# Kernel optimization log

Hardware: AMD Instinct MI355X
Metric: run time of the kernel (lower is better)

Reference implementation:

```python
import math
import jax, jax.numpy as jnp
import numpy as np

N_HEAD = 16
ROPE_BASE = 10000.0


def _rope_sin_cos(T, head_size, dtype):
    half = head_size // 2
    pos = jnp.arange(T, dtype=jnp.float32)[:, None]                      # [T,1]
    div = jnp.exp(jnp.arange(0, head_size, 2, dtype=jnp.float32) * (-math.log(ROPE_BASE) / head_size))  # [half]
    ang = pos * div                                                       # [T,half]
    return jnp.sin(ang).astype(dtype), jnp.cos(ang).astype(dtype)


def _apply_rope(q, k, sin, cos):
    # q,k: [B,T,H,D]; sin,cos: [T,D/2] -> broadcast [1,T,1,D/2]
    half = q.shape[-1] // 2
    sin = sin[None, :, None, :]
    cos = cos[None, :, None, :]
    q1, q2 = q[..., :half], q[..., half:]
    k1, k2 = k[..., :half], k[..., half:]
    q_rot = jnp.concatenate([q1 * cos - q2 * sin, q2 * cos + q1 * sin], axis=-1)
    k_rot = jnp.concatenate([k1 * cos - k2 * sin, k2 * cos + k1 * sin], axis=-1)
    return q_rot, k_rot


def setup_inputs() -> dict:
    key = jax.random.key(0)
    k1, k2, k3 = jax.random.split(key, 3)
    B, T, C = 2, 2048, 2048
    x = jax.random.normal(k1, (B, T, C), dtype=jnp.float32)
    qkv_w = jax.random.normal(k2, (3 * C, C), dtype=jnp.float32) * 0.02
    out_w = jax.random.normal(k3, (C, C), dtype=jnp.float32) * 0.02
    return {"x": x, "qkv_w": qkv_w, "out_w": out_w}


def reference(x, qkv_w, out_w):
    B, T, C = x.shape
    H = N_HEAD
    D = C // H
    qkv = (x @ qkv_w.T).reshape(B, T, 3, H, D)
    q, k, v = qkv[:, :, 0], qkv[:, :, 1], qkv[:, :, 2]   # [B,T,H,D]
    sin, cos = _rope_sin_cos(T, D, x.dtype)
    q, k = _apply_rope(q, k, sin, cos)
    scale = 1.0 / math.sqrt(D)
    scores = jnp.einsum('bthd,bshd->bhts', q, k) * scale  # [B,H,T,T]
    causal = jnp.tril(jnp.ones((T, T), dtype=bool))
    scores = jnp.where(causal[None, None], scores, jnp.finfo(scores.dtype).min)
    probs = jax.nn.softmax(scores, axis=-1)
    attn = jnp.einsum('bhts,bshd->bthd', probs, v)        # [B,T,H,D] (flash output layout)
    # Faithful to original: view(B,T,H,D).permute(0,2,1,3).reshape(B,T,C)
    attn = jnp.transpose(attn, (0, 2, 1, 3)).reshape(B, T, C)
    return attn @ out_w.T
```

## Files before the change

kernel.cpp:

```cpp
#include <hip/hip_runtime.h>

typedef __attribute__((ext_vector_type(8))) short short8;
typedef __attribute__((ext_vector_type(4))) float f32x4;

#define GLOAD16(g, l) __builtin_amdgcn_global_load_lds(                         \
    (const __attribute__((address_space(1))) void*)(g),                          \
    (__attribute__((address_space(3))) void*)(l), 16, 0, 0)

__device__ __forceinline__ float bf2f(unsigned short u) {
  union { unsigned int i; float f; } c; c.i = ((unsigned int)u) << 16; return c.f;
}
__device__ __forceinline__ unsigned short f2bf(float f) {
  union { float f; unsigned int i; } c; c.f = f;
  unsigned int u = c.i;
  u = (u + 0x7fffu + ((u >> 16) & 1u)) >> 16;
  return (unsigned short)u;
}

__global__ __launch_bounds__(256) void cvt_f32_bf16(const float* __restrict__ src,
                                                    unsigned short* __restrict__ dst,
                                                    int n8) {
  int i = blockIdx.x * 256 + threadIdx.x;
  if (i >= n8) return;
  const float4* s4 = (const float4*)src + (long)i * 2;
  float4 a = s4[0], b = s4[1];
  short8 o;
  o[0] = (short)f2bf(a.x); o[1] = (short)f2bf(a.y);
  o[2] = (short)f2bf(a.z); o[3] = (short)f2bf(a.w);
  o[4] = (short)f2bf(b.x); o[5] = (short)f2bf(b.y);
  o[6] = (short)f2bf(b.z); o[7] = (short)f2bf(b.w);
  *((short8*)dst + i) = o;
}

template<int OUT_F32>
__global__ __launch_bounds__(256) void gemm_bt(const unsigned short* __restrict__ A,
                                               const unsigned short* __restrict__ B,
                                               void* __restrict__ Cout,
                                               int M, int N, int K) {
  __shared__ __attribute__((aligned(16))) unsigned short Ah[128 * 64];
  __shared__ __attribute__((aligned(16))) unsigned short Bh[128 * 64];
  const int tid = threadIdx.x;
  const int l = tid & 63;
  const int w = tid >> 6;
  const int wm = w >> 1, wn = w & 1;
  const long brow = (long)blockIdx.y * 128;
  const long bcol = (long)blockIdx.x * 128;

  f32x4 acc[4][4];
#pragma unroll
  for (int i = 0; i < 4; ++i)
#pragma unroll
    for (int j = 0; j < 4; ++j) acc[i][j] = (f32x4){0.f, 0.f, 0.f, 0.f};

  const int srow = tid >> 3;
  const int sg = tid & 7;
  const int lwb = w << 10;

  for (int k0 = 0; k0 < K; k0 += 64) {
    __syncthreads();
#pragma unroll
    for (int i = 0; i < 4; ++i) {
      const int r = srow + i * 32;
      const int gp = (sg ^ (r & 7)) * 8;
      GLOAD16(A + (brow + r) * K + k0 + gp, (char*)Ah + lwb + i * 4096);
      GLOAD16(B + (bcol + r) * K + k0 + gp, (char*)Bh + lwb + i * 4096);
    }
    __syncthreads();
#pragma unroll
    for (int ks = 0; ks < 2; ++ks) {
      short8 af[4], bf[4];
#pragma unroll
      for (int mi = 0; mi < 4; ++mi) {
        const int row = wm * 64 + mi * 16 + (l & 15);
        const int byt = (row * 128 + (l >> 4) * 16 + ks * 64) ^ ((row & 7) << 4);
        af[mi] = *(const short8*)((const char*)Ah + byt);
      }
#pragma unroll
      for (int nj = 0; nj < 4; ++nj) {
        const int row = wn * 64 + nj * 16 + (l & 15);
        const int byt = (row * 128 + (l >> 4) * 16 + ks * 64) ^ ((row & 7) << 4);
        bf[nj] = *(const short8*)((const char*)Bh + byt);
      }
#pragma unroll
      for (int mi = 0; mi < 4; ++mi)
#pragma unroll
        for (int nj = 0; nj < 4; ++nj)
          acc[mi][nj] = __builtin_amdgcn_mfma_f32_16x16x32_bf16(af[mi], bf[nj],
                                                                acc[mi][nj], 0, 0, 0);
    }
  }

  const long rb = brow + wm * 64 + (l >> 4) * 4;
  const long cb = bcol + wn * 64 + (l & 15);
#pragma unroll
  for (int mi = 0; mi < 4; ++mi)
#pragma unroll
    for (int nj = 0; nj < 4; ++nj)
#pragma unroll
      for (int j = 0; j < 4; ++j) {
        const long row = rb + mi * 16 + j;
        const long col = cb + nj * 16;
        if (OUT_F32) ((float*)Cout)[row * N + col] = acc[mi][nj][j];
        else ((unsigned short*)Cout)[row * N + col] = f2bf(acc[mi][nj][j]);
      }
}

__global__ __launch_bounds__(256) void rope_qk(unsigned short* __restrict__ qkv) {
  int gid = blockIdx.x * 256 + threadIdx.x;
  int m = gid >> 10;
  int h = (gid >> 6) & 15;
  int d = gid & 63;
  int t = m & 2047;
  long base = (long)m * 6144 + h * 128;
  float inv = expf(-(float)(2 * d) * 0.07195578415606394f);
  float ang = (float)t * inv;
  float s = sinf(ang), c = cosf(ang);
  float q1 = bf2f(qkv[base + d]),        q2 = bf2f(qkv[base + 64 + d]);
  qkv[base + d]        = f2bf(q1 * c - q2 * s);
  qkv[base + 64 + d]   = f2bf(q2 * c + q1 * s);
  float k1 = bf2f(qkv[base + 2048 + d]), k2 = bf2f(qkv[base + 2048 + 64 + d]);
  qkv[base + 2048 + d]      = f2bf(k1 * c - k2 * s);
  qkv[base + 2048 + 64 + d] = f2bf(k2 * c + k1 * s);
}

__global__ __launch_bounds__(256) void transpose_v(const unsigned short* __restrict__ qkv,
                                                   unsigned short* __restrict__ vt) {
  __shared__ __attribute__((aligned(16))) unsigned short tile[32][136];
  int tid = threadIdx.x;
  int t0 = blockIdx.x * 32;
  int bh = blockIdx.y;
  int b = bh >> 4, h = bh & 15;
  {
    int tt = tid >> 3;
    int dcb = (tid & 7) * 16;
    const unsigned short* src = qkv + (long)(b * 2048 + t0 + tt) * 6144 + 4096 + h * 128 + dcb;
    *(short8*)&tile[tt][dcb]     = *(const short8*)src;
    *(short8*)&tile[tt][dcb + 8] = *(const short8*)(src + 8);
  }
  __syncthreads();
  {
    int d = tid >> 1;
    int ts = (tid & 1) * 16;
    short8 o0, o1;
#pragma unroll
    for (int i = 0; i < 8; ++i) o0[i] = (short)tile[ts + i][d];
#pragma unroll
    for (int i = 0; i < 8; ++i) o1[i] = (short)tile[ts + 8 + i][d];
    unsigned short* dst = vt + (long)bh * 262144 + (long)d * 2048 + t0 + ts;
    *(short8*)dst       = o0;
    *(short8*)(dst + 8) = o1;
  }
}

#define LOG2E 1.4426950408889634f
__global__ __launch_bounds__(256) void flash_attn(const unsigned short* __restrict__ qkv,
                                                  const unsigned short* __restrict__ vt,
                                                  unsigned short* __restrict__ attn) {
  __shared__ __attribute__((aligned(16))) unsigned short Kh[64 * 128];
  __shared__ __attribute__((aligned(16))) unsigned short Vh[128 * 64];
  __shared__ __attribute__((aligned(16))) unsigned short Ph[4][16 * 64];

  const int tid = threadIdx.x;
  const int l = tid & 63;
  const int w = tid >> 6;
  const int qt = (int)(gridDim.x - 1) - (int)blockIdx.x;
  const int bh = blockIdx.y;
  const int b = bh >> 4, h = bh & 15;
  const int q0 = qt * 64;
  const float scale = 0.08838834764831845f;

  short8 qf[4];
  {
    const int qrow = q0 + w * 16 + (l & 15);
    const unsigned short* qp = qkv + (long)(b * 2048 + qrow) * 6144 + h * 128 + (l >> 4) * 8;
#pragma unroll
    for (int dc = 0; dc < 4; ++dc) {
      short8 v = *(const short8*)(qp + dc * 32);
#pragma unroll
      for (int j = 0; j < 8; ++j) v[j] = (short)f2bf(bf2f((unsigned short)v[j]) * scale);
      qf[dc] = v;
    }
  }

  f32x4 accO[8];
#pragma unroll
  for (int i = 0; i < 8; ++i) accO[i] = (f32x4){0.f, 0.f, 0.f, 0.f};
  float mrow[4], lrow[4];
#pragma unroll
  for (int j = 0; j < 4; ++j) { mrow[j] = -INFINITY; lrow[j] = 0.f; }

  const int kvEnd = q0 + 64;
  for (int kv0 = 0; kv0 < kvEnd; kv0 += 64) {
    __syncthreads();
#pragma unroll
    for (int i = 0; i < 4; ++i) {
      const int kr = (tid >> 4) + i * 16;
      const int kgp = ((tid & 15) ^ (kr & 7)) * 8;
      GLOAD16(qkv + (long)(b * 2048 + kv0 + kr) * 6144 + 2048 + h * 128 + kgp,
              (char*)Kh + (w << 10) + i * 4096);
      const int vr = (tid >> 3) + i * 32;
      const int vgp = ((tid & 7) ^ (vr & 7)) * 8;
      GLOAD16(vt + (long)bh * 262144 + (long)vr * 2048 + kv0 + vgp,
              (char*)Vh + (w << 10) + i * 4096);
    }
    __syncthreads();

    f32x4 s[4];
#pragma unroll
    for (int kvt = 0; kvt < 4; ++kvt) {
      s[kvt] = (f32x4){0.f, 0.f, 0.f, 0.f};
#pragma unroll
      for (int dc = 0; dc < 4; ++dc) {
        const int krow = kvt * 16 + (l & 15);
        const int byt = (krow * 256 + (l >> 4) * 16 + dc * 64) ^ ((krow & 7) << 4);
        short8 kf = *(const short8*)((const char*)Kh + byt);
        s[kvt] = __builtin_amdgcn_mfma_f32_16x16x32_bf16(qf[dc], kf, s[kvt], 0, 0, 0);
      }
    }

    const int qrc = q0 + w * 16 + ((l >> 4) << 2);
    float mx[4];
#pragma unroll
    for (int j = 0; j < 4; ++j) mx[j] = -1e30f;
#pragma unroll
    for (int kvt = 0; kvt < 4; ++kvt) {
      const int kvcol = kv0 + kvt * 16 + (l & 15);
#pragma unroll
      for (int j = 0; j < 4; ++j) {
        float sv = s[kvt][j];
        if (kvcol > qrc + j) sv = -1e30f;
        s[kvt][j] = sv;
        mx[j] = fmaxf(mx[j], sv);
      }
    }
#pragma unroll
    for (int j = 0; j < 4; ++j) {
      float v = mx[j];
      v = fmaxf(v, __shfl_xor(v, 1));
      v = fmaxf(v, __shfl_xor(v, 2));
      v = fmaxf(v, __shfl_xor(v, 4));
      v = fmaxf(v, __shfl_xor(v, 8));
      mx[j] = v;
    }
    float alpha[4];
#pragma unroll
    for (int j = 0; j < 4; ++j) {
      float mnew = fmaxf(mrow[j], mx[j]);
      alpha[j] = exp2f((mrow[j] - mnew) * LOG2E);
      mrow[j] = mnew;
    }
    float ps[4] = {0.f, 0.f, 0.f, 0.f};
#pragma unroll
    for (int kvt = 0; kvt < 4; ++kvt) {
#pragma unroll
      for (int j = 0; j < 4; ++j) {
        float p = exp2f((s[kvt][j] - mrow[j]) * LOG2E);
        ps[j] += p;
        const int prow = ((l >> 4) << 2) + j;
        const int pcol = kvt * 16 + (l & 15);
        const int byt = (prow * 128 + pcol * 2) ^ ((prow & 7) << 4);
        *(unsigned short*)((char*)&Ph[w][0] + byt) = f2bf(p);
      }
    }
#pragma unroll
    for (int j = 0; j < 4; ++j) {
      float v = ps[j];
      v += __shfl_xor(v, 1);
      v += __shfl_xor(v, 2);
      v += __shfl_xor(v, 4);
      v += __shfl_xor(v, 8);
      lrow[j] = lrow[j] * alpha[j] + v;
    }
    __syncthreads();

#pragma unroll
    for (int dn = 0; dn < 8; ++dn)
#pragma unroll
      for (int j = 0; j < 4; ++j) accO[dn][j] *= alpha[j];
#pragma unroll
    for (int half = 0; half < 2; ++half) {
      const int prow = (l & 15);
      const int pbyt = (prow * 128 + (l >> 4) * 16 + half * 64) ^ ((prow & 7) << 4);
      short8 pf = *(const short8*)((const char*)&Ph[w][0] + pbyt);
#pragma unroll
      for (int dn = 0; dn < 8; ++dn) {
        const int vrow = dn * 16 + (l & 15);
        const int vbyt = (vrow * 128 + (l >> 4) * 16 + half * 64) ^ ((vrow & 7) << 4);
        short8 vf = *(const short8*)((const char*)Vh + vbyt);
        accO[dn] = __builtin_amdgcn_mfma_f32_16x16x32_bf16(pf, vf, accO[dn], 0, 0, 0);
      }
    }
  }

#pragma unroll
  for (int dn = 0; dn < 8; ++dn)
#pragma unroll
    for (int j = 0; j < 4; ++j) {
      const int qrow = q0 + w * 16 + ((l >> 4) << 2) + j;
      const int d = dn * 16 + (l & 15);
      attn[((long)bh * 2048 + qrow) * 128 + d] = f2bf(accO[dn][j] / lrow[j]);
    }
}

extern "C" void kernel_launch(void* const* d_in, const int* in_sizes, int n_in,
                              void* d_out, int out_size, void* d_ws, size_t ws_size,
                              hipStream_t stream) {
  (void)in_sizes; (void)n_in; (void)out_size; (void)ws_size;
  const float* x  = (const float*)d_in[0];
  const float* qw = (const float*)d_in[1];
  const float* ow = (const float*)d_in[2];
  float* out = (float*)d_out;
  char* ws = (char*)d_ws;

  unsigned short* xb    = (unsigned short*)(ws + 0);
  unsigned short* wqb   = (unsigned short*)(ws + 16777216);
  unsigned short* qkvb  = (unsigned short*)(ws + 41943040);
  unsigned short* vtb   = (unsigned short*)(ws + 0);
  unsigned short* attnb = (unsigned short*)(ws + 16777216);
  unsigned short* wob   = (unsigned short*)(ws + 33554432);

  cvt_f32_bf16<<<4096, 256, 0, stream>>>(x, xb, 1048576);
  cvt_f32_bf16<<<6144, 256, 0, stream>>>(qw, wqb, 1572864);
  gemm_bt<0><<<dim3(48, 32), 256, 0, stream>>>(xb, wqb, (void*)qkvb, 4096, 6144, 2048);
  cvt_f32_bf16<<<2048, 256, 0, stream>>>(ow, wob, 524288);
  rope_qk<<<16384, 256, 0, stream>>>(qkvb);
  transpose_v<<<dim3(64, 32), 256, 0, stream>>>(qkvb, vtb);
  flash_attn<<<dim3(32, 32), 256, 0, stream>>>(qkvb, vtb, attnb);
  gemm_bt<1><<<dim3(16, 32), 256, 0, stream>>>(attnb, wob, (void*)out, 4096, 2048, 2048);
}
```

Baseline: 505.5 us.

## Pair causal query tiles per block, double-buffer K/V, and table-based vectorized RoPE

Each flash-attention block now handles two query tiles, tile qtA and its mirror 31-qtA. The two tiles share K/V loads and balance the causal work across blocks. K/V staging is double-buffered: the next tile is prefetched with global_load_lds while the current one is computed, which leaves one __syncthreads per iteration. log2e is folded into the Q scale, so the per-element exp multiplies go away. RoPE now reads a precomputed sin/cos table with 8-wide vector loads instead of calling sin, cos and exp for every element. Register pressure grows from carrying two accumulator sets, and LDS use roughly doubles.

```diff
diff --git a/kernel.cpp b/kernel.cpp
--- a/kernel.cpp
+++ b/kernel.cpp
@@ -105,22 +105,51 @@
       }
 }
 
-__global__ __launch_bounds__(256) void rope_qk(unsigned short* __restrict__ qkv) {
+__global__ __launch_bounds__(256) void sincos_tab(float* __restrict__ tab) {
   int gid = blockIdx.x * 256 + threadIdx.x;
-  int m = gid >> 10;
-  int h = (gid >> 6) & 15;
-  int d = gid & 63;
-  int t = m & 2047;
-  long base = (long)m * 6144 + h * 128;
+  int t = gid >> 6, d = gid & 63;
   float inv = expf(-(float)(2 * d) * 0.07195578415606394f);
   float ang = (float)t * inv;
-  float s = sinf(ang), c = cosf(ang);
-  float q1 = bf2f(qkv[base + d]),        q2 = bf2f(qkv[base + 64 + d]);
-  qkv[base + d]        = f2bf(q1 * c - q2 * s);
-  qkv[base + 64 + d]   = f2bf(q2 * c + q1 * s);
-  float k1 = bf2f(qkv[base + 2048 + d]), k2 = bf2f(qkv[base + 2048 + 64 + d]);
-  qkv[base + 2048 + d]      = f2bf(k1 * c - k2 * s);
-  qkv[base + 2048 + 64 + d] = f2bf(k2 * c + k1 * s);
+  tab[2 * gid]     = sinf(ang);
+  tab[2 * gid + 1] = cosf(ang);
+}
+
+__global__ __launch_bounds__(256) void rope_qk(unsigned short* __restrict__ qkv,
+                                               const float* __restrict__ tab) {
+  int gid = blockIdx.x * 256 + threadIdx.x;
+  int m = gid >> 7;
+  int h = (gid >> 3) & 15;
+  int db = gid & 7;
+  int t = m & 2047;
+  long base = (long)m * 6144 + h * 128 + db * 8;
+  const float* tp = tab + ((long)(t << 6) + db * 8) * 2;
+  float4 t0 = *(const float4*)(tp + 0);
+  float4 t1 = *(const float4*)(tp + 4);
+  float4 t2 = *(const float4*)(tp + 8);
+  float4 t3 = *(const float4*)(tp + 12);
+  float sj[8] = {t0.x, t0.z, t1.x, t1.z, t2.x, t2.z, t3.x, t3.z};
+  float cj[8] = {t0.y, t0.w, t1.y, t1.w, t2.y, t2.w, t3.y, t3.w};
+
+  unsigned short* qp = qkv + base;
+  short8 q1 = *(short8*)qp, q2 = *(short8*)(qp + 64);
+  short8 o1, o2;
+#pragma unroll
+  for (int j = 0; j < 8; ++j) {
+    float a = bf2f((unsigned short)q1[j]), bq = bf2f((unsigned short)q2[j]);
+    o1[j] = (short)f2bf(a * cj[j] - bq * sj[j]);
+    o2[j] = (short)f2bf(bq * cj[j] + a * sj[j]);
+  }
+  *(short8*)qp = o1; *(short8*)(qp + 64) = o2;
+
+  unsigned short* kp = qkv + base + 2048;
+  short8 k1 = *(short8*)kp, k2 = *(short8*)(kp + 64);
+#pragma unroll
+  for (int j = 0; j < 8; ++j) {
+    float a = bf2f((unsigned short)k1[j]), bk = bf2f((unsigned short)k2[j]);
+    o1[j] = (short)f2bf(a * cj[j] - bk * sj[j]);
+    o2[j] = (short)f2bf(bk * cj[j] + a * sj[j]);
+  }
+  *(short8*)kp = o1; *(short8*)(kp + 64) = o2;
 }
 
 __global__ __launch_bounds__(256) void transpose_v(const unsigned short* __restrict__ qkv,
@@ -152,153 +181,176 @@
   }
 }
 
-#define LOG2E 1.4426950408889634f
-__global__ __launch_bounds__(256) void flash_attn(const unsigned short* __restrict__ qkv,
-                                                  const unsigned short* __restrict__ vt,
-                                                  unsigned short* __restrict__ attn) {
-  __shared__ __attribute__((aligned(16))) unsigned short Kh[64 * 128];
-  __shared__ __attribute__((aligned(16))) unsigned short Vh[128 * 64];
-  __shared__ __attribute__((aligned(16))) unsigned short Ph[4][16 * 64];
+#define STAGE(IT, BUF) do {                                                     \
+    const int kv0s_ = (IT) * 64;                                                \
+    _Pragma("unroll")                                                           \
+    for (int i_ = 0; i_ < 4; ++i_) {                                            \
+      const int kr_ = (tid >> 4) + i_ * 16;                                     \
+      const int kgp_ = ((tid & 15) ^ (kr_ & 7)) * 8;                            \
+      GLOAD16(qkv + (long)(b * 2048 + kv0s_ + kr_) * 6144 + 2048 + h * 128 + kgp_, \
+              (char*)&Kh[BUF][0] + (w << 10) + i_ * 4096);                      \
+      const int vr_ = (tid >> 3) + i_ * 32;                                     \
+      const int vgp_ = ((tid & 7) ^ (vr_ & 7)) * 8;                             \
+      GLOAD16(vt + (long)bh * 262144 + (long)vr_ * 2048 + kv0s_ + vgp_,         \
+              (char*)&Vh[BUF][0] + (w << 10) + i_ * 4096);                      \
+    }                                                                           \
+  } while (0)
+
+#define COMPUTE_TILE(QF, ACC, MR, LR, Q0, PHP, BUFB) do {                       \
+    f32x4 s_[4];                                                                \
+    _Pragma("unroll")                                                           \
+    for (int kvt_ = 0; kvt_ < 4; ++kvt_) {                                      \
+      s_[kvt_] = (f32x4){0.f, 0.f, 0.f, 0.f};                                   \
+      _Pragma("unroll")                                                         \
+      for (int dc_ = 0; dc_ < 4; ++dc_) {                                       \
+        const int krow_ = kvt_ * 16 + (l & 15);                                 \
+        const int byt_ = ((krow_ * 256 + (l >> 4) * 16 + dc_ * 64)              \
+                          ^ ((krow_ & 7) << 4)) + (BUFB);                       \
+        short8 kf_ = *(const short8*)((const char*)Kh + byt_);                  \
+        s_[kvt_] = __builtin_amdgcn_mfma_f32_16x16x32_bf16(QF[dc_], kf_,        \
+                                                           s_[kvt_], 0, 0, 0);  \
+      }                                                                         \
+    }                                                                           \
+    const int qrc_ = (Q0) + w * 16 + ((l >> 4) << 2);                           \
+    float mx_[4];                                                               \
+    _Pragma("unroll") for (int j_ = 0; j_ < 4; ++j_) mx_[j_] = -1e30f;          \
+    _Pragma("unroll")                                                           \
+    for (int kvt_ = 0; kvt_ < 4; ++kvt_) {                                      \
+      const int kvcol_ = kv0 + kvt_ * 16 + (l & 15);                            \
+      _Pragma("unroll")                                                         \
+      for (int j_ = 0; j_ < 4; ++j_) {                                          \
+        float sv_ = s_[kvt_][j_];                                               \
+        if (kvcol_ > qrc_ + j_) sv_ = -1e30f;                                   \
+        s_[kvt_][j_] = sv_;                                                     \
+        mx_[j_] = fmaxf(mx_[j_], sv_);                                          \
+      }                                                                         \
+    }                                                                           \
+    float alpha_[4];                                                            \
+    _Pragma("unroll")                                                           \
+    for (int j_ = 0; j_ < 4; ++j_) {                                            \
+      float v_ = mx_[j_];                                                       \
+      v_ = fmaxf(v_, __shfl_xor(v_, 1));                                        \
+      v_ = fmaxf(v_, __shfl_xor(v_, 2));                                        \
+      v_ = fmaxf(v_, __shfl_xor(v_, 4));                                        \
+      v_ = fmaxf(v_, __shfl_xor(v_, 8));                                        \
+      float mnew_ = fmaxf((MR)[j_], v_);                                        \
+      alpha_[j_] = exp2f((MR)[j_] - mnew_);                                     \
+      (MR)[j_] = mnew_;                                                         \
+    }                                                                           \
+    float ps_[4] = {0.f, 0.f, 0.f, 0.f};                                        \
+    _Pragma("unroll")                                                           \
+    for (int kvt_ = 0; kvt_ < 4; ++kvt_) {                                      \
+      _Pragma("unroll")                                                         \
+      for (int j_ = 0; j_ < 4; ++j_) {                                          \
+        float p_ = exp2f(s_[kvt_][j_] - (MR)[j_]);                              \
+        ps_[j_] += p_;                                                          \
+        const int prow_ = ((l >> 4) << 2) + j_;                                 \
+        const int pcol_ = kvt_ * 16 + (l & 15);                                 \
+        const int pb_ = (prow_ * 128 + pcol_ * 2) ^ ((prow_ & 7) << 4);         \
+        *(unsigned short*)((char*)(PHP) + pb_) = f2bf(p_);                      \
+      }                                                                         \
+    }                                                                           \
+    _Pragma("unroll")                                                           \
+    for (int j_ = 0; j_ < 4; ++j_) {                                            \
+      float v_ = ps_[j_];                                                       \
+      v_ += __shfl_xor(v_, 1);                                                  \
+      v_ += __shfl_xor(v_, 2);                                                  \
+      v_ += __shfl_xor(v_, 4);                                                  \
+      v_ += __shfl_xor(v_, 8);                                                  \
+      (LR)[j_] = (LR)[j_] * alpha_[j_] + v_;                                    \
+    }                                                                           \
+    asm volatile("s_waitcnt lgkmcnt(0)" ::: "memory");                          \
+    __builtin_amdgcn_sched_barrier(0);                                          \
+    _Pragma("unroll")                                                           \
+    for (int dn_ = 0; dn_ < 8; ++dn_)                                           \
+      _Pragma("unroll")                                                         \
+      for (int j_ = 0; j_ < 4; ++j_) (ACC)[dn_][j_] *= alpha_[j_];              \
+    _Pragma("unroll")                                                           \
+    for (int half_ = 0; half_ < 2; ++half_) {                                   \
+      const int prw_ = (l & 15);                                                \
+      const int pb_ = (prw_ * 128 + (l >> 4) * 16 + half_ * 64)                 \
+                      ^ ((prw_ & 7) << 4);                                      \
+      short8 pf_ = *(const short8*)((const char*)(PHP) + pb_);                  \
+      _Pragma("unroll")                                                         \
+      for (int dn_ = 0; dn_ < 8; ++dn_) {                                       \
+        const int vrow_ = dn_ * 16 + (l & 15);                                  \
+        const int vb_ = ((vrow_ * 128 + (l >> 4) * 16 + half_ * 64)             \
+                         ^ ((vrow_ & 7) << 4)) + (BUFB);                        \
+        short8 vf_ = *(const short8*)((const char*)Vh + vb_);                   \
+        (ACC)[dn_] = __builtin_amdgcn_mfma_f32_16x16x32_bf16(pf_, vf_,          \
+                                                             (ACC)[dn_], 0, 0, 0); \
+      }                                                                         \
+    }                                                                           \
+  } while (0)
+
+__global__ __launch_bounds__(256, 2) void flash_attn(const unsigned short* __restrict__ qkv,
+                                                     const unsigned short* __restrict__ vt,
+                                                     unsigned short* __restrict__ attn) {
+  __shared__ __attribute__((aligned(16))) unsigned short Kh[2][64 * 128];
+  __shared__ __attribute__((aligned(16))) unsigned short Vh[2][128 * 64];
+  __shared__ __attribute__((aligned(16))) unsigned short Ph[4][2][16 * 64];
 
   const int tid = threadIdx.x;
   const int l = tid & 63;
   const int w = tid >> 6;
-  const int qt = (int)(gridDim.x - 1) - (int)blockIdx.x;
   const int bh = blockIdx.y;
   const int b = bh >> 4, h = bh & 15;
-  const int q0 = qt * 64;
-  const float scale = 0.08838834764831845f;
-
-  short8 qf[4];
+  const int qtA = blockIdx.x;
+  const int qtB = 31 - qtA;
+  const int q0A = qtA * 64, q0B = qtB * 64;
+  const int endA = q0A + 64;
+  const int nIter = qtB + 1;
+  const float qscale = 0.08838834764831845f * 1.4426950408889634f;
+
+  short8 qfA[4], qfB[4];
   {
-    const int qrow = q0 + w * 16 + (l & 15);
-    const unsigned short* qp = qkv + (long)(b * 2048 + qrow) * 6144 + h * 128 + (l >> 4) * 8;
+    const int qrA = q0A + w * 16 + (l & 15);
+    const int qrB = q0B + w * 16 + (l & 15);
+    const unsigned short* qpA = qkv + (long)(b * 2048 + qrA) * 6144 + h * 128 + (l >> 4) * 8;
+    const unsigned short* qpB = qkv + (long)(b * 2048 + qrB) * 6144 + h * 128 + (l >> 4) * 8;
 #pragma unroll
     for (int dc = 0; dc < 4; ++dc) {
-      short8 v = *(const short8*)(qp + dc * 32);
-#pragma unroll
-      for (int j = 0; j < 8; ++j) v[j] = (short)f2bf(bf2f((unsigned short)v[j]) * scale);
-      qf[dc] = v;
+      short8 va = *(const short8*)(qpA + dc * 32);
+      short8 vb = *(const short8*)(qpB + dc * 32);
+#pragma unroll
+      for (int j = 0; j < 8; ++j) {
+        va[j] = (short)f2bf(bf2f((unsigned short)va[j]) * qscale);
+        vb[j] = (short)f2bf(bf2f((unsigned short)vb[j]) * qscale);
+      }
+      qfA[dc] = va; qfB[dc] = vb;
     }
   }
 
-  f32x4 accO[8];
-#pragma unroll
-  for (int i = 0; i < 8; ++i) accO[i] = (f32x4){0.f, 0.f, 0.f, 0.f};
-  float mrow[4], lrow[4];
-#pragma unroll
-  for (int j = 0; j < 4; ++j) { mrow[j] = -INFINITY; lrow[j] = 0.f; }
-
-  const int kvEnd = q0 + 64;
-  for (int kv0 = 0; kv0 < kvEnd; kv0 += 64) {
+  f32x4 accA[8], accB[8];
+#pragma unroll
+  for (int i = 0; i < 8; ++i) {
+    accA[i] = (f32x4){0.f, 0.f, 0.f, 0.f};
+    accB[i] = (f32x4){0.f, 0.f, 0.f, 0.f};
+  }
+  float mA[4], lA[4], mB[4], lB[4];
+#pragma unroll
+  for (int j = 0; j < 4; ++j) { mA[j] = -INFINITY; lA[j] = 0.f; mB[j] = -INFINITY; lB[j] = 0.f; }
+
+  STAGE(0, 0);
+  __syncthreads();
+  for (int it = 0; it < nIter; ++it) {
+    const int kv0 = it * 64;
+    if (it + 1 < nIter) STAGE(it + 1, (it + 1) & 1);
+    const int bufb = (it & 1) * 16384;
+    COMPUTE_TILE(qfB, accB, mB, lB, q0B, (char*)&Ph[w][0][0], bufb);
+    if (kv0 < endA) COMPUTE_TILE(qfA, accA, mA, lA, q0A, (char*)&Ph[w][1][0], bufb);
     __syncthreads();
-#pragma unroll
-    for (int i = 0; i < 4; ++i) {
-      const int kr = (tid >> 4) + i * 16;
-      const int kgp = ((tid & 15) ^ (kr & 7)) * 8;
-      GLOAD16(qkv + (long)(b * 2048 + kv0 + kr) * 6144 + 2048 + h * 128 + kgp,
-              (char*)Kh + (w << 10) + i * 4096);
-      const int vr = (tid >> 3) + i * 32;
-      const int vgp = ((tid & 7) ^ (vr & 7)) * 8;
-      GLOAD16(vt + (long)bh * 262144 + (long)vr * 2048 + kv0 + vgp,
-              (char*)Vh + (w << 10) + i * 4096);
-    }
-    __syncthreads();
-
-    f32x4 s[4];
-#pragma unroll
-    for (int kvt = 0; kvt < 4; ++kvt) {
-      s[kvt] = (f32x4){0.f, 0.f, 0.f, 0.f};
-#pragma unroll
-      for (int dc = 0; dc < 4; ++dc) {
-        const int krow = kvt * 16 + (l & 15);
-        const int byt = (krow * 256 + (l >> 4) * 16 + dc * 64) ^ ((krow & 7) << 4);
-        short8 kf = *(const short8*)((const char*)Kh + byt);
-        s[kvt] = __builtin_amdgcn_mfma_f32_16x16x32_bf16(qf[dc], kf, s[kvt], 0, 0, 0);
-      }
-    }
-
-    const int qrc = q0 + w * 16 + ((l >> 4) << 2);
-    float mx[4];
-#pragma unroll
-    for (int j = 0; j < 4; ++j) mx[j] = -1e30f;
-#pragma unroll
-    for (int kvt = 0; kvt < 4; ++kvt) {
-      const int kvcol = kv0 + kvt * 16 + (l & 15);
-#pragma unroll
-      for (int j = 0; j < 4; ++j) {
-        float sv = s[kvt][j];
-        if (kvcol > qrc + j) sv = -1e30f;
-        s[kvt][j] = sv;
-        mx[j] = fmaxf(mx[j], sv);
-      }
-    }
+  }
+
+#pragma unroll
+  for (int dn = 0; dn < 8; ++dn)
 #pragma unroll
     for (int j = 0; j < 4; ++j) {
-      float v = mx[j];
-      v = fmaxf(v, __shfl_xor(v, 1));
-      v = fmaxf(v, __shfl_xor(v, 2));
-      v = fmaxf(v, __shfl_xor(v, 4));
-      v = fmaxf(v, __shfl_xor(v, 8));
-      mx[j] = v;
-    }
-    float alpha[4];
-#pragma unroll
-    for (int j = 0; j < 4; ++j) {
-      float mnew = fmaxf(mrow[j], mx[j]);
-      alpha[j] = exp2f((mrow[j] - mnew) * LOG2E);
-      mrow[j] = mnew;
-    }
-    float ps[4] = {0.f, 0.f, 0.f, 0.f};
-#pragma unroll
-    for (int kvt = 0; kvt < 4; ++kvt) {
-#pragma unroll
-      for (int j = 0; j < 4; ++j) {
-        float p = exp2f((s[kvt][j] - mrow[j]) * LOG2E);
-        ps[j] += p;
-        const int prow = ((l >> 4) << 2) + j;
-        const int pcol = kvt * 16 + (l & 15);
-        const int byt = (prow * 128 + pcol * 2) ^ ((prow & 7) << 4);
-        *(unsigned short*)((char*)&Ph[w][0] + byt) = f2bf(p);
-      }
-    }
-#pragma unroll
-    for (int j = 0; j < 4; ++j) {
-      float v = ps[j];
-      v += __shfl_xor(v, 1);
-      v += __shfl_xor(v, 2);
-      v += __shfl_xor(v, 4);
-      v += __shfl_xor(v, 8);
-      lrow[j] = lrow[j] * alpha[j] + v;
-    }
-    __syncthreads();
-
-#pragma unroll
-    for (int dn = 0; dn < 8; ++dn)
-#pragma unroll
-      for (int j = 0; j < 4; ++j) accO[dn][j] *= alpha[j];
-#pragma unroll
-    for (int half = 0; half < 2; ++half) {
-      const int prow = (l & 15);
-      const int pbyt = (prow * 128 + (l >> 4) * 16 + half * 64) ^ ((prow & 7) << 4);
-      short8 pf = *(const short8*)((const char*)&Ph[w][0] + pbyt);
-#pragma unroll
-      for (int dn = 0; dn < 8; ++dn) {
-        const int vrow = dn * 16 + (l & 15);
-        const int vbyt = (vrow * 128 + (l >> 4) * 16 + half * 64) ^ ((vrow & 7) << 4);
-        short8 vf = *(const short8*)((const char*)Vh + vbyt);
-        accO[dn] = __builtin_amdgcn_mfma_f32_16x16x32_bf16(pf, vf, accO[dn], 0, 0, 0);
-      }
-    }
-  }
-
-#pragma unroll
-  for (int dn = 0; dn < 8; ++dn)
-#pragma unroll
-    for (int j = 0; j < 4; ++j) {
-      const int qrow = q0 + w * 16 + ((l >> 4) << 2) + j;
+      const int qrowB = q0B + w * 16 + ((l >> 4) << 2) + j;
+      const int qrowA = q0A + w * 16 + ((l >> 4) << 2) + j;
       const int d = dn * 16 + (l & 15);
-      attn[((long)bh * 2048 + qrow) * 128 + d] = f2bf(accO[dn][j] / lrow[j]);
+      attn[((long)bh * 2048 + qrowB) * 128 + d] = f2bf(accB[dn][j] / lB[j]);
+      attn[((long)bh * 2048 + qrowA) * 128 + d] = f2bf(accA[dn][j] / lA[j]);
     }
 }
 
@@ -315,6 +367,7 @@
   unsigned short* xb    = (unsigned short*)(ws + 0);
   unsigned short* wqb   = (unsigned short*)(ws + 16777216);
   unsigned short* qkvb  = (unsigned short*)(ws + 41943040);
+  float*          tabf  = (float*)(ws + 0);
   unsigned short* vtb   = (unsigned short*)(ws + 0);
   unsigned short* attnb = (unsigned short*)(ws + 16777216);
   unsigned short* wob   = (unsigned short*)(ws + 33554432);
@@ -322,9 +375,10 @@
   cvt_f32_bf16<<<4096, 256, 0, stream>>>(x, xb, 1048576);
   cvt_f32_bf16<<<6144, 256, 0, stream>>>(qw, wqb, 1572864);
   gemm_bt<0><<<dim3(48, 32), 256, 0, stream>>>(xb, wqb, (void*)qkvb, 4096, 6144, 2048);
+  sincos_tab<<<512, 256, 0, stream>>>(tabf);
   cvt_f32_bf16<<<2048, 256, 0, stream>>>(ow, wob, 524288);
-  rope_qk<<<16384, 256, 0, stream>>>(qkvb);
+  rope_qk<<<2048, 256, 0, stream>>>(qkvb, tabf);
   transpose_v<<<dim3(64, 32), 256, 0, stream>>>(qkvb, vtb);
-  flash_attn<<<dim3(32, 32), 256, 0, stream>>>(qkvb, vtb, attnb);
+  flash_attn<<<dim3(16, 32), 256, 0, stream>>>(qkvb, vtb, attnb);
   gemm_bt<1><<<dim3(16, 32), 256, 0, stream>>>(attnb, wob, (void*)out, 4096, 2048, 2048);
 }
```

New measurement: 428.7 us. -15.2%, faster.
